# Kernel tuning notes

Hardware: AMD Instinct MI355X
Metric: run time of the kernel (lower is better)

The kernel has to match this reference:

```python
import jax, jax.numpy as jnp
import numpy as np

B = 1048576  # number of Gaussians
EPS = 1e-8


def setup_inputs() -> dict:
    key = jax.random.key(0)
    ks = jax.random.split(key, 6)
    return {
        "loc1": jax.random.normal(ks[0], (B, 3), dtype=jnp.float32),
        "scale1": jax.random.uniform(ks[1], (B, 3), dtype=jnp.float32),
        "rot_matrix1": jax.random.normal(ks[2], (B, 3, 3), dtype=jnp.float32),
        "loc2": jax.random.normal(ks[3], (B, 3), dtype=jnp.float32),
        "scale2": jax.random.uniform(ks[4], (B, 3), dtype=jnp.float32),
        "rot_matrix2": jax.random.normal(ks[5], (B, 3, 3), dtype=jnp.float32),
    }


def reference(loc1, scale1, rot_matrix1, loc2, scale2, rot_matrix2):
    # Wasserstein-2 distance between batched 3D Gaussians.
    scale1 = jnp.clip(scale1, EPS)
    scale2 = jnp.clip(scale2, EPS)

    loc_diff2 = jnp.sum((loc1 - loc2) ** 2, axis=-1)  # [B]

    # cov2 = R2 diag(scale2) R2^T  -> [B,3,3]
    cov2 = jnp.einsum('bij,bj,bkj->bik', rot_matrix2, scale2, rot_matrix2)

    # cov2 rotated into frame 1: R1^T cov2 R1
    cov2_R1 = jnp.einsum('bji,bjk,bkl->bil', rot_matrix1, cov2, rot_matrix1)

    # E = diag(sqrt(scale1)) cov2_R1 diag(sqrt(scale1)), symmetrized
    s1_sqrt = jnp.sqrt(scale1)  # [B,3]
    E = s1_sqrt[:, :, None] * cov2_R1 * s1_sqrt[:, None, :]
    E = 0.5 * (E + jnp.swapaxes(E, -1, -2)) + EPS * jnp.eye(3, dtype=E.dtype)

    eigs = jnp.clip(jnp.linalg.eigvalsh(E), EPS)  # [B,3]
    E_sqrt_trace = jnp.sqrt(eigs).sum(axis=-1)  # [B]

    cov_w = (scale1.sum(axis=-1)
             + jnp.einsum('bii->b', cov2)
             - 2.0 * E_sqrt_trace)
    cov_w = jnp.clip(cov_w, 0.0)

    return jnp.sqrt(jnp.clip(loc_diff2 + cov_w, EPS))
```

## Files before the change

### kernel.cpp

```cpp
#include <hip/hip_runtime.h>
#include <math.h>

#define EPSF 1e-8f

__global__ __launch_bounds__(256) void wasserstein_kernel(
    const float* __restrict__ loc1, const float* __restrict__ scale1,
    const float* __restrict__ rot1, const float* __restrict__ loc2,
    const float* __restrict__ scale2, const float* __restrict__ rot2,
    float* __restrict__ out, int B)
{
    int i = blockIdx.x * blockDim.x + threadIdx.x;
    if (i >= B) return;

    const float* l1 = loc1 + 3 * i;
    const float* l2 = loc2 + 3 * i;
    const float* s1p = scale1 + 3 * i;
    const float* s2p = scale2 + 3 * i;
    const float* R1p = rot1 + 9 * i;
    const float* R2p = rot2 + 9 * i;

    float s1[3], s2[3];
#pragma unroll
    for (int k = 0; k < 3; k++) {
        s1[k] = fmaxf(s1p[k], EPSF);
        s2[k] = fmaxf(s2p[k], EPSF);
    }

    float R1[3][3], R2[3][3];
#pragma unroll
    for (int r = 0; r < 3; r++)
#pragma unroll
        for (int c = 0; c < 3; c++) {
            R1[r][c] = R1p[3 * r + c];
            R2[r][c] = R2p[3 * r + c];
        }

    float d0 = l1[0] - l2[0];
    float d1 = l1[1] - l2[1];
    float d2 = l1[2] - l2[2];
    float loc_diff2 = d0 * d0 + d1 * d1 + d2 * d2;

    float cov2[3][3];
    float tr_cov2 = 0.0f;
#pragma unroll
    for (int r = 0; r < 3; r++) {
#pragma unroll
        for (int c = r; c < 3; c++) {
            float acc = 0.0f;
#pragma unroll
            for (int j = 0; j < 3; j++)
                acc += R2[r][j] * s2[j] * R2[c][j];
            cov2[r][c] = acc;
            cov2[c][r] = acc;
        }
        tr_cov2 += cov2[r][r];
    }

    float T[3][3];
#pragma unroll
    for (int r = 0; r < 3; r++)
#pragma unroll
        for (int c = 0; c < 3; c++) {
            float acc = 0.0f;
#pragma unroll
            for (int j = 0; j < 3; j++)
                acc += cov2[r][j] * R1[j][c];
            T[r][c] = acc;
        }

    float M[3][3];
#pragma unroll
    for (int r = 0; r < 3; r++)
#pragma unroll
        for (int c = 0; c < 3; c++) {
            float acc = 0.0f;
#pragma unroll
            for (int j = 0; j < 3; j++)
                acc += R1[j][r] * T[j][c];
            M[r][c] = acc;
        }

    float ss0 = sqrtf(s1[0]), ss1 = sqrtf(s1[1]), ss2 = sqrtf(s1[2]);
    double a00 = (double)(s1[0] * M[0][0]) + 1e-8;
    double a11 = (double)(s1[1] * M[1][1]) + 1e-8;
    double a22 = (double)(s1[2] * M[2][2]) + 1e-8;
    double a01 = (double)(0.5f * (M[0][1] + M[1][0]) * ss0 * ss1);
    double a02 = (double)(0.5f * (M[0][2] + M[2][0]) * ss0 * ss2);
    double a12 = (double)(0.5f * (M[1][2] + M[2][1]) * ss1 * ss2);

    double q = (a00 + a11 + a22) * (1.0 / 3.0);
    double b00 = a00 - q, b11 = a11 - q, b22 = a22 - q;
    double p1 = a01 * a01 + a02 * a02 + a12 * a12;
    double p2 = b00 * b00 + b11 * b11 + b22 * b22 + 2.0 * p1;

    double e0, e1, e2;
    if (p2 <= 1e-30) {
        e0 = q; e1 = q; e2 = q;
    } else {
        double p = sqrt(p2 * (1.0 / 6.0));
        double invp = 1.0 / p;
        double c00 = b00 * invp, c11 = b11 * invp, c22 = b22 * invp;
        double c01 = a01 * invp, c02 = a02 * invp, c12 = a12 * invp;
        double detB = c00 * (c11 * c22 - c12 * c12)
                    - c01 * (c01 * c22 - c12 * c02)
                    + c02 * (c01 * c12 - c11 * c02);
        double r = 0.5 * detB;
        r = fmin(1.0, fmax(-1.0, r));
        double phi = acos(r) * (1.0 / 3.0);
        double twop = 2.0 * p;
        e0 = q + twop * cos(phi);
        e2 = q + twop * cos(phi + 2.0943951023931953);
        e1 = 3.0 * q - e0 - e2;
    }

    double eps_d = 1e-8;
    double tr_sqrt = sqrt(fmax(e0, eps_d)) + sqrt(fmax(e1, eps_d)) + sqrt(fmax(e2, eps_d));

    float cov_w = (s1[0] + s1[1] + s1[2]) + tr_cov2 - 2.0f * (float)tr_sqrt;
    cov_w = fmaxf(cov_w, 0.0f);

    out[i] = sqrtf(fmaxf(loc_diff2 + cov_w, EPSF));
}

extern "C" void kernel_launch(void* const* d_in, const int* in_sizes, int n_in,
                              void* d_out, int out_size, void* d_ws, size_t ws_size,
                              hipStream_t stream) {
    const float* loc1   = (const float*)d_in[0];
    const float* scale1 = (const float*)d_in[1];
    const float* rot1   = (const float*)d_in[2];
    const float* loc2   = (const float*)d_in[3];
    const float* scale2 = (const float*)d_in[4];
    const float* rot2   = (const float*)d_in[5];
    float* out = (float*)d_out;

    int B = in_sizes[0] / 3;
    int block = 256;
    int grid = (B + block - 1) / block;
    wasserstein_kernel<<<grid, block, 0, stream>>>(loc1, scale1, rot1, loc2, scale2, rot2, out, B);
}
```

Measured before the change: 150.5 us.

## Process four Gaussians per thread with float4 vectorized loads and stores

Each thread now handles four consecutive Gaussians, loading loc, scale and rotation data as aligned float4 vectors and writing results as one float4. This replaces the stride-3 and stride-9 scalar loads, which coalesce poorly, with wide contiguous loads. The eigenvalue solve moves into an inlined helper. It raises register pressure (36-float rotation arrays held per thread, plus double-precision math) and cuts the thread count by four, which may reduce occupancy. It also assumes B is divisible by four, silently dropping any tail elements otherwise.

```diff
diff --git a/kernel.cpp b/kernel.cpp
--- a/kernel.cpp
+++ b/kernel.cpp
@@ -3,91 +3,9 @@
 
 #define EPSF 1e-8f
 
-__global__ __launch_bounds__(256) void wasserstein_kernel(
-    const float* __restrict__ loc1, const float* __restrict__ scale1,
-    const float* __restrict__ rot1, const float* __restrict__ loc2,
-    const float* __restrict__ scale2, const float* __restrict__ rot2,
-    float* __restrict__ out, int B)
+__device__ __forceinline__ double tr_sqrt_eig(double a00, double a11, double a22,
+                                              double a01, double a02, double a12)
 {
-    int i = blockIdx.x * blockDim.x + threadIdx.x;
-    if (i >= B) return;
-
-    const float* l1 = loc1 + 3 * i;
-    const float* l2 = loc2 + 3 * i;
-    const float* s1p = scale1 + 3 * i;
-    const float* s2p = scale2 + 3 * i;
-    const float* R1p = rot1 + 9 * i;
-    const float* R2p = rot2 + 9 * i;
-
-    float s1[3], s2[3];
-#pragma unroll
-    for (int k = 0; k < 3; k++) {
-        s1[k] = fmaxf(s1p[k], EPSF);
-        s2[k] = fmaxf(s2p[k], EPSF);
-    }
-
-    float R1[3][3], R2[3][3];
-#pragma unroll
-    for (int r = 0; r < 3; r++)
-#pragma unroll
-        for (int c = 0; c < 3; c++) {
-            R1[r][c] = R1p[3 * r + c];
-            R2[r][c] = R2p[3 * r + c];
-        }
-
-    float d0 = l1[0] - l2[0];
-    float d1 = l1[1] - l2[1];
-    float d2 = l1[2] - l2[2];
-    float loc_diff2 = d0 * d0 + d1 * d1 + d2 * d2;
-
-    float cov2[3][3];
-    float tr_cov2 = 0.0f;
-#pragma unroll
-    for (int r = 0; r < 3; r++) {
-#pragma unroll
-        for (int c = r; c < 3; c++) {
-            float acc = 0.0f;
-#pragma unroll
-            for (int j = 0; j < 3; j++)
-                acc += R2[r][j] * s2[j] * R2[c][j];
-            cov2[r][c] = acc;
-            cov2[c][r] = acc;
-        }
-        tr_cov2 += cov2[r][r];
-    }
-
-    float T[3][3];
-#pragma unroll
-    for (int r = 0; r < 3; r++)
-#pragma unroll
-        for (int c = 0; c < 3; c++) {
-            float acc = 0.0f;
-#pragma unroll
-            for (int j = 0; j < 3; j++)
-                acc += cov2[r][j] * R1[j][c];
-            T[r][c] = acc;
-        }
-
-    float M[3][3];
-#pragma unroll
-    for (int r = 0; r < 3; r++)
-#pragma unroll
-        for (int c = 0; c < 3; c++) {
-            float acc = 0.0f;
-#pragma unroll
-            for (int j = 0; j < 3; j++)
-                acc += R1[j][r] * T[j][c];
-            M[r][c] = acc;
-        }
-
-    float ss0 = sqrtf(s1[0]), ss1 = sqrtf(s1[1]), ss2 = sqrtf(s1[2]);
-    double a00 = (double)(s1[0] * M[0][0]) + 1e-8;
-    double a11 = (double)(s1[1] * M[1][1]) + 1e-8;
-    double a22 = (double)(s1[2] * M[2][2]) + 1e-8;
-    double a01 = (double)(0.5f * (M[0][1] + M[1][0]) * ss0 * ss1);
-    double a02 = (double)(0.5f * (M[0][2] + M[2][0]) * ss0 * ss2);
-    double a12 = (double)(0.5f * (M[1][2] + M[2][1]) * ss1 * ss2);
-
     double q = (a00 + a11 + a22) * (1.0 / 3.0);
     double b00 = a00 - q, b11 = a11 - q, b22 = a22 - q;
     double p1 = a01 * a01 + a02 * a02 + a12 * a12;
@@ -112,14 +30,134 @@
         e2 = q + twop * cos(phi + 2.0943951023931953);
         e1 = 3.0 * q - e0 - e2;
     }
+    double eps_d = 1e-8;
+    return sqrt(fmax(e0, eps_d)) + sqrt(fmax(e1, eps_d)) + sqrt(fmax(e2, eps_d));
+}
 
-    double eps_d = 1e-8;
-    double tr_sqrt = sqrt(fmax(e0, eps_d)) + sqrt(fmax(e1, eps_d)) + sqrt(fmax(e2, eps_d));
+__global__ __launch_bounds__(256) void wasserstein_kernel(
+    const float* __restrict__ loc1, const float* __restrict__ scale1,
+    const float* __restrict__ rot1, const float* __restrict__ loc2,
+    const float* __restrict__ scale2, const float* __restrict__ rot2,
+    float* __restrict__ out, int B4)
+{
+    int t = blockIdx.x * blockDim.x + threadIdx.x;
+    if (t >= B4) return;
 
-    float cov_w = (s1[0] + s1[1] + s1[2]) + tr_cov2 - 2.0f * (float)tr_sqrt;
-    cov_w = fmaxf(cov_w, 0.0f);
+    const float4* l1p = (const float4*)loc1   + 3 * t;
+    const float4* l2p = (const float4*)loc2   + 3 * t;
+    const float4* s1p = (const float4*)scale1 + 3 * t;
+    const float4* s2p = (const float4*)scale2 + 3 * t;
+    const float4* r1p = (const float4*)rot1   + 9 * t;
+    const float4* r2p = (const float4*)rot2   + 9 * t;
 
-    out[i] = sqrtf(fmaxf(loc_diff2 + cov_w, EPSF));
+    float loc_diff2[4];
+    {
+        float L1[12], L2[12];
+#pragma unroll
+        for (int k = 0; k < 3; k++) {
+            float4 a = l1p[k], b = l2p[k];
+            L1[4 * k + 0] = a.x; L1[4 * k + 1] = a.y; L1[4 * k + 2] = a.z; L1[4 * k + 3] = a.w;
+            L2[4 * k + 0] = b.x; L2[4 * k + 1] = b.y; L2[4 * k + 2] = b.z; L2[4 * k + 3] = b.w;
+        }
+#pragma unroll
+        for (int g = 0; g < 4; g++) {
+            float d0 = L1[3 * g + 0] - L2[3 * g + 0];
+            float d1 = L1[3 * g + 1] - L2[3 * g + 1];
+            float d2 = L1[3 * g + 2] - L2[3 * g + 2];
+            loc_diff2[g] = d0 * d0 + d1 * d1 + d2 * d2;
+        }
+    }
+
+    float cov2[4][6];
+    float tr_cov2[4];
+    {
+        float S2[12], R2[36];
+#pragma unroll
+        for (int k = 0; k < 3; k++) {
+            float4 v = s2p[k];
+            S2[4 * k + 0] = v.x; S2[4 * k + 1] = v.y; S2[4 * k + 2] = v.z; S2[4 * k + 3] = v.w;
+        }
+#pragma unroll
+        for (int k = 0; k < 9; k++) {
+            float4 v = r2p[k];
+            R2[4 * k + 0] = v.x; R2[4 * k + 1] = v.y; R2[4 * k + 2] = v.z; R2[4 * k + 3] = v.w;
+        }
+#pragma unroll
+        for (int g = 0; g < 4; g++) {
+            float s0 = fmaxf(S2[3 * g + 0], EPSF);
+            float s1 = fmaxf(S2[3 * g + 1], EPSF);
+            float s2 = fmaxf(S2[3 * g + 2], EPSF);
+            const float* R = R2 + 9 * g;
+            float c00 = R[0] * s0 * R[0] + R[1] * s1 * R[1] + R[2] * s2 * R[2];
+            float c11 = R[3] * s0 * R[3] + R[4] * s1 * R[4] + R[5] * s2 * R[5];
+            float c22 = R[6] * s0 * R[6] + R[7] * s1 * R[7] + R[8] * s2 * R[8];
+            float c01 = R[0] * s0 * R[3] + R[1] * s1 * R[4] + R[2] * s2 * R[5];
+            float c02 = R[0] * s0 * R[6] + R[1] * s1 * R[7] + R[2] * s2 * R[8];
+            float c12 = R[3] * s0 * R[6] + R[4] * s1 * R[7] + R[5] * s2 * R[8];
+            cov2[g][0] = c00; cov2[g][1] = c11; cov2[g][2] = c22;
+            cov2[g][3] = c01; cov2[g][4] = c02; cov2[g][5] = c12;
+            tr_cov2[g] = c00 + c11 + c22;
+        }
+    }
+
+    float res[4];
+    {
+        float S1[12], R1[36];
+#pragma unroll
+        for (int k = 0; k < 3; k++) {
+            float4 v = s1p[k];
+            S1[4 * k + 0] = v.x; S1[4 * k + 1] = v.y; S1[4 * k + 2] = v.z; S1[4 * k + 3] = v.w;
+        }
+#pragma unroll
+        for (int k = 0; k < 9; k++) {
+            float4 v = r1p[k];
+            R1[4 * k + 0] = v.x; R1[4 * k + 1] = v.y; R1[4 * k + 2] = v.z; R1[4 * k + 3] = v.w;
+        }
+#pragma unroll
+        for (int g = 0; g < 4; g++) {
+            float s0 = fmaxf(S1[3 * g + 0], EPSF);
+            float s1 = fmaxf(S1[3 * g + 1], EPSF);
+            float s2 = fmaxf(S1[3 * g + 2], EPSF);
+            const float* R = R1 + 9 * g;
+            float C[3][3];
+            C[0][0] = cov2[g][0]; C[1][1] = cov2[g][1]; C[2][2] = cov2[g][2];
+            C[0][1] = C[1][0] = cov2[g][3];
+            C[0][2] = C[2][0] = cov2[g][4];
+            C[1][2] = C[2][1] = cov2[g][5];
+
+            float T[3][3];
+#pragma unroll
+            for (int r = 0; r < 3; r++)
+#pragma unroll
+                for (int c = 0; c < 3; c++)
+                    T[r][c] = C[r][0] * R[c] + C[r][1] * R[3 + c] + C[r][2] * R[6 + c];
+
+            float M[3][3];
+#pragma unroll
+            for (int r = 0; r < 3; r++)
+#pragma unroll
+                for (int c = 0; c < 3; c++)
+                    M[r][c] = R[r] * T[0][c] + R[3 + r] * T[1][c] + R[6 + r] * T[2][c];
+
+            float ss0 = sqrtf(s0), ss1 = sqrtf(s1), ss2 = sqrtf(s2);
+            double a00 = (double)(s0 * M[0][0]) + 1e-8;
+            double a11 = (double)(s1 * M[1][1]) + 1e-8;
+            double a22 = (double)(s2 * M[2][2]) + 1e-8;
+            double a01 = (double)(0.5f * (M[0][1] + M[1][0]) * ss0 * ss1);
+            double a02 = (double)(0.5f * (M[0][2] + M[2][0]) * ss0 * ss2);
+            double a12 = (double)(0.5f * (M[1][2] + M[2][1]) * ss1 * ss2);
+
+            double trs = tr_sqrt_eig(a00, a11, a22, a01, a02, a12);
+
+            float cov_w = (s0 + s1 + s2) + tr_cov2[g] - 2.0f * (float)trs;
+            cov_w = fmaxf(cov_w, 0.0f);
+            res[g] = sqrtf(fmaxf(loc_diff2[g] + cov_w, EPSF));
+        }
+    }
+
+    float4 o;
+    o.x = res[0]; o.y = res[1]; o.z = res[2]; o.w = res[3];
+    ((float4*)out)[t] = o;
 }
 
 extern "C" void kernel_launch(void* const* d_in, const int* in_sizes, int n_in,
@@ -134,7 +172,8 @@
     float* out = (float*)d_out;
 
     int B = in_sizes[0] / 3;
+    int B4 = B / 4;
     int block = 256;
-    int grid = (B + block - 1) / block;
-    wasserstein_kernel<<<grid, block, 0, stream>>>(loc1, scale1, rot1, loc2, scale2, rot2, out, B);
+    int grid = (B4 + block - 1) / block;
+    wasserstein_kernel<<<grid, block, 0, stream>>>(loc1, scale1, rot1, loc2, scale2, rot2, out, B4);
 }
```

After: 157.9 us. 1.05x slower.
